# Kernel optimization log

Hardware: AMD Instinct MI355X
Metric: run time of the kernel (lower is better)

Reference implementation:

```python
import jax, jax.numpy as jnp
import numpy as np

N_NODES = 50000


def _glorot(key, fan_in, fan_out):
    limit = float(np.sqrt(6.0 / (fan_in + fan_out)))
    return jax.random.uniform(key, (fan_in, fan_out), jnp.float32, -limit, limit)


def setup_inputs() -> dict:
    key = jax.random.key(0)
    k_x, k_src, k_dst, k1, k2, k3 = jax.random.split(key, 6)
    x = jax.random.normal(k_x, (N_NODES, 128), dtype=jnp.float32)
    src = jax.random.randint(k_src, (800000,), 0, N_NODES)
    dst = jax.random.randint(k_dst, (800000,), 0, N_NODES)
    edge_index = jnp.stack([src, dst]).astype(jnp.int64)  # [2, E]
    W1 = _glorot(k1, 128, 96)
    W2 = _glorot(k2, 96, 96)
    W3 = _glorot(k3, 96, 40)
    b1 = jnp.zeros((96,), jnp.float32)
    b2 = jnp.zeros((96,), jnp.float32)
    b3 = jnp.zeros((40,), jnp.float32)
    return {"x": x, "W1": W1, "b1": b1, "W2": W2, "b2": b2,
            "W3": W3, "b3": b3, "edge_index": edge_index}


def _aggregate(x, src, dst):
    # sparse adj SpMM with 'add' reduce: out[dst] += x[src]
    return jax.ops.segment_sum(x[src], dst, num_segments=N_NODES)


def reference(x, W1, b1, W2, b2, W3, b3, edge_index):
    src, dst = edge_index[0], edge_index[1]
    # layer 1: aggregate -> linear -> relu (dropout identity in eval)
    h = jax.nn.relu(_aggregate(x, src, dst) @ W1 + b1)
    # layer 2
    h = jax.nn.relu(_aggregate(h, src, dst) @ W2 + b2)
    # layer 3 + log_softmax
    logits = _aggregate(h, src, dst) @ W3 + b3
    return jax.nn.log_softmax(logits, axis=-1)
```

## Files before the change

kernel.cpp:

```cpp
#include <hip/hip_runtime.h>
#include <math.h>

typedef __attribute__((ext_vector_type(8))) short bf16x8;
typedef __attribute__((ext_vector_type(4))) float f32x4;

__device__ __forceinline__ unsigned short f2bf(float f) {
  unsigned u = __float_as_uint(f);
  u += 0x7fffu + ((u >> 16) & 1u);
  return (unsigned short)(u >> 16);
}
__device__ __forceinline__ float bflo(unsigned u) { return __uint_as_float(u << 16); }
__device__ __forceinline__ float bfhi(unsigned u) { return __uint_as_float(u & 0xffff0000u); }


constexpr int CB = 64;

__global__ __launch_bounds__(256) void bucket_count(const int* __restrict__ dst,
                                                    int* __restrict__ partial, int E) {
  __shared__ int bkt[256];
  int tid = threadIdx.x;
  bkt[tid] = 0;
  __syncthreads();
  int E4 = E >> 2;
  const int4* d4 = (const int4*)dst;
  for (int i = blockIdx.x * 256 + tid; i < E4; i += gridDim.x * 256) {
    int4 d = d4[i];
    atomicAdd(&bkt[d.x >> 8], 1);
    atomicAdd(&bkt[d.y >> 8], 1);
    atomicAdd(&bkt[d.z >> 8], 1);
    atomicAdd(&bkt[d.w >> 8], 1);
  }
  if (blockIdx.x == 0 && tid < (E & 3)) atomicAdd(&bkt[dst[E4 * 4 + tid] >> 8], 1);
  __syncthreads();
  partial[blockIdx.x * 256 + tid] = bkt[tid];
}

__global__ __launch_bounds__(256) void scan_pack(const int* __restrict__ partial,
                                                 int* __restrict__ gstart, int* __restrict__ gcur,
                                                 int* __restrict__ row_ptr,
                                                 const float* __restrict__ W1,
                                                 const float* __restrict__ W2,
                                                 const float* __restrict__ W3,
                                                 unsigned short* __restrict__ Wp1,
                                                 unsigned short* __restrict__ Wp2,
                                                 unsigned short* __restrict__ Wp3,
                                                 int NB, int N, int E) {
  if (blockIdx.x == 0) {
    int tid = threadIdx.x;
    int s = 0;
#pragma unroll 8
    for (int i = 0; i < CB; ++i) s += partial[i * 256 + tid];
    __shared__ int sm[256];
    sm[tid] = s;
    __syncthreads();
    for (int off = 1; off < 256; off <<= 1) {
      int u = (tid >= off) ? sm[tid - off] : 0;
      __syncthreads();
      sm[tid] += u;
      __syncthreads();
    }
    int excl = sm[tid] - s;
    if (tid < NB) { gstart[tid] = excl; gcur[tid] = excl; }
    if (tid == NB - 1) gstart[NB] = sm[tid];
    if (tid == 0) row_ptr[N] = E;
    return;
  }
  int gid = (blockIdx.x - 1) * 256 + threadIdx.x;
  const float* W;
  unsigned short* Wp;
  int t, NCTT, M, MV;
  if (gid < 1536) {
    W = W1; Wp = Wp1; t = gid; NCTT = 6; M = 96; MV = 96;
  } else if (gid < 2688) {
    W = W2; Wp = Wp2; t = gid - 1536; NCTT = 6; M = 96; MV = 96;
  } else if (gid < 3264) {
    W = W3; Wp = Wp3; t = gid - 2688; NCTT = 3; M = 40; MV = 40;
  } else {
    return;
  }
  int lane = t & 63;
  int frag = t >> 6;
  int s = frag / NCTT;
  int ct = frag - s * NCTT;
  int colv = ct * 16 + (lane & 15);
  int k0 = s * 32 + (lane >> 4) * 8;
  union { unsigned short s[8]; uint4 u; } pk;
#pragma unroll
  for (int j = 0; j < 8; ++j) {
    float v = (colv < MV) ? W[(k0 + j) * M + colv] : 0.f;
    pk.s[j] = f2bf(v);
  }
  ((uint4*)Wp)[t] = pk.u;
}

__global__ __launch_bounds__(512) void bin_edges(const int* __restrict__ src,
                                                 const int* __restrict__ dst,
                                                 int* __restrict__ gcur,
                                                 int* __restrict__ packed, int E, int NB) {
  __shared__ int lcnt[256];
  __shared__ int gbase[256];
  int tid = threadIdx.x;
  if (tid < 256) lcnt[tid] = 0;
  __syncthreads();
  int idx = blockIdx.x * 512 + tid;
  int E4 = E >> 2;
  int sv[4], dv[4], lv[4];
  int cnt = 0;
  if (idx < E4) {
    int4 s4 = ((const int4*)src)[idx];
    int4 d4 = ((const int4*)dst)[idx];
    sv[0] = s4.x; sv[1] = s4.y; sv[2] = s4.z; sv[3] = s4.w;
    dv[0] = d4.x; dv[1] = d4.y; dv[2] = d4.z; dv[3] = d4.w;
    cnt = 4;
  } else if (idx == E4 && (E & 3)) {
    int tl = E & 3;
    for (int i = 0; i < tl; ++i) { sv[i] = src[E4 * 4 + i]; dv[i] = dst[E4 * 4 + i]; }
    cnt = tl;
  }
  for (int i = 0; i < cnt; ++i) lv[i] = atomicAdd(&lcnt[dv[i] >> 8], 1);
  __syncthreads();
  if (tid < NB) gbase[tid] = atomicAdd(&gcur[tid], lcnt[tid]);
  __syncthreads();
  for (int i = 0; i < cnt; ++i) {
    int b = dv[i] >> 8;
    packed[gbase[b] + lv[i]] = ((dv[i] & 255) << 16) | (sv[i] & 0xffff);
  }
}

__global__ __launch_bounds__(256) void build_local_csr(const int* __restrict__ packed,
                                                       const int* __restrict__ gstart,
                                                       int* __restrict__ row_ptr,
                                                       int* __restrict__ col, int N) {
  __shared__ int cnt[256];
  __shared__ int sm[256];
  int b = blockIdx.x, tid = threadIdx.x;
  int gs = gstart[b], ge = gstart[b + 1];
  int me = ge - gs;
  int node0 = b << 8;
  int RL = N - node0;
  if (RL > 256) RL = 256;
  cnt[tid] = 0;
  __syncthreads();
  for (int i = tid; i < me; i += 256) atomicAdd(&cnt[packed[gs + i] >> 16], 1);
  __syncthreads();
  int v = cnt[tid];
  sm[tid] = v;
  __syncthreads();
  for (int off = 1; off < 256; off <<= 1) {
    int u = (tid >= off) ? sm[tid - off] : 0;
    __syncthreads();
    sm[tid] += u;
    __syncthreads();
  }
  int excl = gs + sm[tid] - v;
  __syncthreads();
  cnt[tid] = excl;
  if (tid < RL) row_ptr[node0 + tid] = excl;
  __syncthreads();
  for (int i = tid; i < me; i += 256) {
    int pk = packed[gs + i];
    int p = atomicAdd(&cnt[pk >> 16], 1);
    col[p] = pk & 0xffff;
  }
}


template <int KSTEPS, int NCTT, bool AF32, bool OUTBF16, int MOUT, int MVALID>
__global__ __launch_bounds__(256) void mfma_gemm(const void* __restrict__ Aptr,
                                                 const unsigned short* __restrict__ Wp,
                                                 void* __restrict__ outp, int N) {
  constexpr int NCT = 3;
  constexpr int K = KSTEPS * 32;
  int wid = threadIdx.x >> 6;
  int lane = threadIdx.x & 63;
  int rt = blockIdx.x * 4 + wid;
  if (rt * 16 >= N) return;
  int g = blockIdx.y;
  int quad = lane >> 4;
  int lm = lane & 15;

  union BU { uint4 u; bf16x8 v; };
  bf16x8 bfrag[KSTEPS][NCT];
  const uint4* wp4 = (const uint4*)Wp;
#pragma unroll
  for (int s = 0; s < KSTEPS; ++s)
#pragma unroll
    for (int c = 0; c < NCT; ++c) {
      BU bu;
      bu.u = wp4[(s * NCTT + g * NCT + c) * 64 + lane];
      bfrag[s][c] = bu.v;
    }

  f32x4 acc[NCT];
#pragma unroll
  for (int c = 0; c < NCT; ++c) acc[c] = (f32x4){0.f, 0.f, 0.f, 0.f};

  int row = rt * 16 + lm;
  if (row >= N) row = N - 1;

#pragma unroll
  for (int s = 0; s < KSTEPS; ++s) {
    int k0 = s * 32 + quad * 8;
    bf16x8 afrag;
    if (AF32) {
      const float* Af = (const float*)Aptr + (size_t)row * K + k0;
      float4 x0 = *(const float4*)(Af);
      float4 x1 = *(const float4*)(Af + 4);
      union { unsigned short s[8]; bf16x8 v; } au;
      au.s[0] = f2bf(x0.x); au.s[1] = f2bf(x0.y); au.s[2] = f2bf(x0.z); au.s[3] = f2bf(x0.w);
      au.s[4] = f2bf(x1.x); au.s[5] = f2bf(x1.y); au.s[6] = f2bf(x1.z); au.s[7] = f2bf(x1.w);
      afrag = au.v;
    } else {
      const unsigned short* Ab = (const unsigned short*)Aptr + (size_t)row * K + k0;
      BU au;
      au.u = *(const uint4*)Ab;
      afrag = au.v;
    }
#pragma unroll
    for (int c = 0; c < NCT; ++c)
      acc[c] = __builtin_amdgcn_mfma_f32_16x16x32_bf16(afrag, bfrag[s][c], acc[c], 0, 0, 0);
  }

#pragma unroll
  for (int c = 0; c < NCT; ++c) {
    int colv = g * 48 + c * 16 + lm;
    if (colv >= MVALID) continue;
#pragma unroll
    for (int r = 0; r < 4; ++r) {
      int orow = rt * 16 + quad * 4 + r;
      if (orow < N) {
        if (OUTBF16)
          ((unsigned short*)outp)[(size_t)orow * MOUT + colv] = f2bf(acc[c][r]);
        else
          ((float*)outp)[(size_t)orow * MOUT + colv] = acc[c][r];
      }
    }
  }
}


__global__ void agg_relu_bf16(const unsigned short* __restrict__ t,
                              const int* __restrict__ row_ptr, const int* __restrict__ col,
                              const float* __restrict__ bias, unsigned short* __restrict__ out,
                              int N) {
  int gid = blockIdx.x * blockDim.x + threadIdx.x;
  int node = gid / 12;
  int c = gid - node * 12;
  if (node >= N) return;
  int beg = row_ptr[node];
  int end = row_ptr[node + 1];
  const unsigned short* tc = t + 8 * c;
  float a0 = 0.f, a1 = 0.f, a2 = 0.f, a3 = 0.f, a4 = 0.f, a5 = 0.f, a6 = 0.f, a7 = 0.f;
  int e = beg;
  for (; e + 1 < end; e += 2) {
    int s0 = col[e], s1 = col[e + 1];
    uint4 u = *(const uint4*)(tc + (size_t)s0 * 96);
    uint4 w = *(const uint4*)(tc + (size_t)s1 * 96);
    a0 += bflo(u.x); a1 += bfhi(u.x);
    a2 += bflo(u.y); a3 += bfhi(u.y);
    a4 += bflo(u.z); a5 += bfhi(u.z);
    a6 += bflo(u.w); a7 += bfhi(u.w);
    a0 += bflo(w.x); a1 += bfhi(w.x);
    a2 += bflo(w.y); a3 += bfhi(w.y);
    a4 += bflo(w.z); a5 += bfhi(w.z);
    a6 += bflo(w.w); a7 += bfhi(w.w);
  }
  if (e < end) {
    int s = col[e];
    uint4 u = *(const uint4*)(tc + (size_t)s * 96);
    a0 += bflo(u.x); a1 += bfhi(u.x);
    a2 += bflo(u.y); a3 += bfhi(u.y);
    a4 += bflo(u.z); a5 += bfhi(u.z);
    a6 += bflo(u.w); a7 += bfhi(u.w);
  }
  const float* b = bias + 8 * c;
  union { unsigned short s[8]; uint4 u; } pk;
  pk.s[0] = f2bf(fmaxf(a0 + b[0], 0.f));
  pk.s[1] = f2bf(fmaxf(a1 + b[1], 0.f));
  pk.s[2] = f2bf(fmaxf(a2 + b[2], 0.f));
  pk.s[3] = f2bf(fmaxf(a3 + b[3], 0.f));
  pk.s[4] = f2bf(fmaxf(a4 + b[4], 0.f));
  pk.s[5] = f2bf(fmaxf(a5 + b[5], 0.f));
  pk.s[6] = f2bf(fmaxf(a6 + b[6], 0.f));
  pk.s[7] = f2bf(fmaxf(a7 + b[7], 0.f));
  *(uint4*)(out + (size_t)node * 96 + 8 * c) = pk.u;
}

__global__ void agg_lsm_bf16(const unsigned short* __restrict__ t,
                             const int* __restrict__ row_ptr, const int* __restrict__ col,
                             const float* __restrict__ bias, float* __restrict__ out, int N) {
  int tid = threadIdx.x;
  int node = blockIdx.x * 16 + (tid >> 4);
  int c = tid & 15;
  bool act = (c < 10) && (node < N);
  int ceff = (c < 10) ? c : 0;
  int beg = 0, end = 0;
  if (node < N) {
    beg = row_ptr[node];
    end = row_ptr[node + 1];
  }
  const unsigned short* tc = t + 4 * ceff;
  float v0 = 0.f, v1 = 0.f, v2 = 0.f, v3 = 0.f;
  if (act) {
    int e = beg;
    for (; e + 1 < end; e += 2) {
      int s0 = col[e], s1 = col[e + 1];
      uint2 u = *(const uint2*)(tc + (size_t)s0 * 40);
      uint2 w = *(const uint2*)(tc + (size_t)s1 * 40);
      v0 += bflo(u.x); v1 += bfhi(u.x);
      v2 += bflo(u.y); v3 += bfhi(u.y);
      v0 += bflo(w.x); v1 += bfhi(w.x);
      v2 += bflo(w.y); v3 += bfhi(w.y);
    }
    if (e < end) {
      int s = col[e];
      uint2 u = *(const uint2*)(tc + (size_t)s * 40);
      v0 += bflo(u.x); v1 += bfhi(u.x);
      v2 += bflo(u.y); v3 += bfhi(u.y);
    }
  }
  const float* bb = bias + 4 * ceff;
  v0 += bb[0]; v1 += bb[1]; v2 += bb[2]; v3 += bb[3];
  float m = act ? fmaxf(fmaxf(v0, v1), fmaxf(v2, v3)) : -__builtin_inff();
#pragma unroll
  for (int off = 8; off; off >>= 1) m = fmaxf(m, __shfl_xor(m, off, 64));
  float ex = act ? (__expf(v0 - m) + __expf(v1 - m) + __expf(v2 - m) + __expf(v3 - m)) : 0.f;
#pragma unroll
  for (int off = 8; off; off >>= 1) ex += __shfl_xor(ex, off, 64);
  if (act) {
    float l = m + __logf(ex);
    float* o = out + (size_t)node * 40 + 4 * c;
    o[0] = v0 - l; o[1] = v1 - l; o[2] = v2 - l; o[3] = v3 - l;
  }
}


extern "C" void kernel_launch(void* const* d_in, const int* in_sizes, int n_in,
                              void* d_out, int out_size, void* d_ws, size_t ws_size,
                              hipStream_t stream) {
  const float* x  = (const float*)d_in[0];
  const float* W1 = (const float*)d_in[1];
  const float* b1 = (const float*)d_in[2];
  const float* W2 = (const float*)d_in[3];
  const float* b2 = (const float*)d_in[4];
  const float* W3 = (const float*)d_in[5];
  const float* b3 = (const float*)d_in[6];
  const int* edge = (const int*)d_in[7];

  int N = in_sizes[0] / 128;
  int E = in_sizes[7] / 2;
  const int* srcp = edge;
  const int* dstp = edge + E;

  char* p = (char*)d_ws;
  auto alloc = [&](size_t bytes) {
    char* r = p;
    p += (bytes + 255) & ~size_t(255);
    return r;
  };
  int NB = (N + 255) >> 8;
  int* partial = (int*)alloc((size_t)CB * 256 * 4);
  int* gstart  = (int*)alloc((size_t)(NB + 1) * 4);
  int* gcur    = (int*)alloc((size_t)NB * 4);
  int* row_ptr = (int*)alloc((size_t)(N + 1) * 4);
  int* packed  = (int*)alloc((size_t)E * 4);
  int* col     = (int*)alloc((size_t)E * 4);
  unsigned short* Wp1 = (unsigned short*)alloc(1536 * 8 * 2);
  unsigned short* Wp2 = (unsigned short*)alloc(1152 * 8 * 2);
  unsigned short* Wp3 = (unsigned short*)alloc(576 * 8 * 2);
  unsigned short* Tb  = (unsigned short*)alloc((size_t)N * 96 * 2);
  unsigned short* Hb  = (unsigned short*)alloc((size_t)N * 96 * 2);
  unsigned short* T3b = (unsigned short*)alloc((size_t)N * 40 * 2);

  bucket_count<<<CB, 256, 0, stream>>>(dstp, partial, E);
  scan_pack<<<14, 256, 0, stream>>>(partial, gstart, gcur, row_ptr,
                                    W1, W2, W3, Wp1, Wp2, Wp3, NB, N, E);
  int E4 = E >> 2;
  int nbin = (E4 + ((E & 3) ? 1 : 0) + 511) / 512;
  bin_edges<<<nbin, 512, 0, stream>>>(srcp, dstp, gcur, packed, E, NB);
  build_local_csr<<<NB, 256, 0, stream>>>(packed, gstart, row_ptr, col, N);

  int rt4 = ((N + 15) / 16 + 3) / 4;
  int aggblocks = (N * 12 + 255) / 256;

  mfma_gemm<4, 6, true, true, 96, 96><<<dim3(rt4, 2), 256, 0, stream>>>(x, Wp1, Tb, N);
  agg_relu_bf16<<<aggblocks, 256, 0, stream>>>(Tb, row_ptr, col, b1, Hb, N);
  mfma_gemm<3, 6, false, true, 96, 96><<<dim3(rt4, 2), 256, 0, stream>>>(Hb, Wp2, Tb, N);
  agg_relu_bf16<<<aggblocks, 256, 0, stream>>>(Tb, row_ptr, col, b2, Hb, N);
  mfma_gemm<3, 3, false, true, 40, 40><<<dim3(rt4, 1), 256, 0, stream>>>(Hb, Wp3, T3b, N);
  agg_lsm_bf16<<<(N + 15) / 16, 256, 0, stream>>>(T3b, row_ptr, col, b3, (float*)d_out, N);
}
```

Measured before the change: 219.6 us.

## Fuse aggregation with next-layer GEMM and merge graph-build kernels with GEMM1

```diff
diff --git a/kernel.cpp b/kernel.cpp
--- a/kernel.cpp
+++ b/kernel.cpp
@@ -15,57 +15,34 @@
 
 constexpr int CB = 64;
 
-__global__ __launch_bounds__(256) void bucket_count(const int* __restrict__ dst,
-                                                    int* __restrict__ partial, int E) {
-  __shared__ int bkt[256];
+__global__ __launch_bounds__(256) void count_pack(const int* __restrict__ dst,
+                                                  int* __restrict__ partial, int E,
+                                                  const float* __restrict__ W1,
+                                                  const float* __restrict__ W2,
+                                                  const float* __restrict__ W3,
+                                                  unsigned short* __restrict__ Wp1,
+                                                  unsigned short* __restrict__ Wp2,
+                                                  unsigned short* __restrict__ Wp3) {
   int tid = threadIdx.x;
-  bkt[tid] = 0;
-  __syncthreads();
-  int E4 = E >> 2;
-  const int4* d4 = (const int4*)dst;
-  for (int i = blockIdx.x * 256 + tid; i < E4; i += gridDim.x * 256) {
-    int4 d = d4[i];
-    atomicAdd(&bkt[d.x >> 8], 1);
-    atomicAdd(&bkt[d.y >> 8], 1);
-    atomicAdd(&bkt[d.z >> 8], 1);
-    atomicAdd(&bkt[d.w >> 8], 1);
-  }
-  if (blockIdx.x == 0 && tid < (E & 3)) atomicAdd(&bkt[dst[E4 * 4 + tid] >> 8], 1);
-  __syncthreads();
-  partial[blockIdx.x * 256 + tid] = bkt[tid];
-}
-
-__global__ __launch_bounds__(256) void scan_pack(const int* __restrict__ partial,
-                                                 int* __restrict__ gstart, int* __restrict__ gcur,
-                                                 int* __restrict__ row_ptr,
-                                                 const float* __restrict__ W1,
-                                                 const float* __restrict__ W2,
-                                                 const float* __restrict__ W3,
-                                                 unsigned short* __restrict__ Wp1,
-                                                 unsigned short* __restrict__ Wp2,
-                                                 unsigned short* __restrict__ Wp3,
-                                                 int NB, int N, int E) {
-  if (blockIdx.x == 0) {
-    int tid = threadIdx.x;
-    int s = 0;
-#pragma unroll 8
-    for (int i = 0; i < CB; ++i) s += partial[i * 256 + tid];
-    __shared__ int sm[256];
-    sm[tid] = s;
-    __syncthreads();
-    for (int off = 1; off < 256; off <<= 1) {
-      int u = (tid >= off) ? sm[tid - off] : 0;
-      __syncthreads();
-      sm[tid] += u;
-      __syncthreads();
-    }
-    int excl = sm[tid] - s;
-    if (tid < NB) { gstart[tid] = excl; gcur[tid] = excl; }
-    if (tid == NB - 1) gstart[NB] = sm[tid];
-    if (tid == 0) row_ptr[N] = E;
+  if (blockIdx.x < CB) {
+    __shared__ int bkt[256];
+    bkt[tid] = 0;
+    __syncthreads();
+    int E4 = E >> 2;
+    const int4* d4 = (const int4*)dst;
+    for (int i = blockIdx.x * 256 + tid; i < E4; i += CB * 256) {
+      int4 d = d4[i];
+      atomicAdd(&bkt[d.x >> 8], 1);
+      atomicAdd(&bkt[d.y >> 8], 1);
+      atomicAdd(&bkt[d.z >> 8], 1);
+      atomicAdd(&bkt[d.w >> 8], 1);
+    }
+    if (blockIdx.x == 0 && tid < (E & 3)) atomicAdd(&bkt[dst[E4 * 4 + tid] >> 8], 1);
+    __syncthreads();
+    partial[blockIdx.x * 256 + tid] = bkt[tid];
     return;
   }
-  int gid = (blockIdx.x - 1) * 256 + threadIdx.x;
+  int gid = (blockIdx.x - CB) * 256 + tid;
   const float* W;
   unsigned short* Wp;
   int t, NCTT, M, MV;
@@ -93,37 +70,112 @@
   ((uint4*)Wp)[t] = pk.u;
 }
 
-__global__ __launch_bounds__(512) void bin_edges(const int* __restrict__ src,
+__global__ __launch_bounds__(256) void scan_kernel(const int* __restrict__ partial,
+                                                   int* __restrict__ gstart,
+                                                   int* __restrict__ gcur,
+                                                   int* __restrict__ row_ptr,
+                                                   int NB, int N, int E) {
+  int tid = threadIdx.x;
+  int s = 0;
+#pragma unroll 8
+  for (int i = 0; i < CB; ++i) s += partial[i * 256 + tid];
+  __shared__ int sm[256];
+  sm[tid] = s;
+  __syncthreads();
+  for (int off = 1; off < 256; off <<= 1) {
+    int u = (tid >= off) ? sm[tid - off] : 0;
+    __syncthreads();
+    sm[tid] += u;
+    __syncthreads();
+  }
+  int excl = sm[tid] - s;
+  if (tid < NB) { gstart[tid] = excl; gcur[tid] = excl; }
+  if (tid == NB - 1) gstart[NB] = sm[tid];
+  if (tid == 0) row_ptr[N] = E;
+}
+
+__global__ __launch_bounds__(256) void bin_gemm1(const int* __restrict__ src,
                                                  const int* __restrict__ dst,
                                                  int* __restrict__ gcur,
-                                                 int* __restrict__ packed, int E, int NB) {
-  __shared__ int lcnt[256];
-  __shared__ int gbase[256];
+                                                 int* __restrict__ packed, int E, int NB,
+                                                 int NBIN, const float* __restrict__ x,
+                                                 const unsigned short* __restrict__ Wp1,
+                                                 unsigned short* __restrict__ Tb, int N) {
   int tid = threadIdx.x;
-  if (tid < 256) lcnt[tid] = 0;
-  __syncthreads();
-  int idx = blockIdx.x * 512 + tid;
-  int E4 = E >> 2;
-  int sv[4], dv[4], lv[4];
-  int cnt = 0;
-  if (idx < E4) {
-    int4 s4 = ((const int4*)src)[idx];
-    int4 d4 = ((const int4*)dst)[idx];
-    sv[0] = s4.x; sv[1] = s4.y; sv[2] = s4.z; sv[3] = s4.w;
-    dv[0] = d4.x; dv[1] = d4.y; dv[2] = d4.z; dv[3] = d4.w;
-    cnt = 4;
-  } else if (idx == E4 && (E & 3)) {
-    int tl = E & 3;
-    for (int i = 0; i < tl; ++i) { sv[i] = src[E4 * 4 + i]; dv[i] = dst[E4 * 4 + i]; }
-    cnt = tl;
-  }
-  for (int i = 0; i < cnt; ++i) lv[i] = atomicAdd(&lcnt[dv[i] >> 8], 1);
-  __syncthreads();
-  if (tid < NB) gbase[tid] = atomicAdd(&gcur[tid], lcnt[tid]);
-  __syncthreads();
-  for (int i = 0; i < cnt; ++i) {
-    int b = dv[i] >> 8;
-    packed[gbase[b] + lv[i]] = ((dv[i] & 255) << 16) | (sv[i] & 0xffff);
+  if (blockIdx.x < NBIN) {
+    __shared__ int lcnt[256];
+    __shared__ int gbase[256];
+    lcnt[tid] = 0;
+    __syncthreads();
+    int idx = blockIdx.x * 256 + tid;
+    int E4 = E >> 2;
+    int sv[4], dv[4], lv[4];
+    int cnt = 0;
+    if (idx < E4) {
+      int4 s4 = ((const int4*)src)[idx];
+      int4 d4 = ((const int4*)dst)[idx];
+      sv[0] = s4.x; sv[1] = s4.y; sv[2] = s4.z; sv[3] = s4.w;
+      dv[0] = d4.x; dv[1] = d4.y; dv[2] = d4.z; dv[3] = d4.w;
+      cnt = 4;
+    } else if (idx == E4 && (E & 3)) {
+      int tl = E & 3;
+      for (int i = 0; i < tl; ++i) { sv[i] = src[E4 * 4 + i]; dv[i] = dst[E4 * 4 + i]; }
+      cnt = tl;
+    }
+    for (int i = 0; i < cnt; ++i) lv[i] = atomicAdd(&lcnt[dv[i] >> 8], 1);
+    __syncthreads();
+    if (tid < NB) gbase[tid] = atomicAdd(&gcur[tid], lcnt[tid]);
+    __syncthreads();
+    for (int i = 0; i < cnt; ++i) {
+      int b = dv[i] >> 8;
+      packed[gbase[b] + lv[i]] = ((dv[i] & 255) << 16) | (sv[i] & 0xffff);
+    }
+    return;
+  }
+  int bx = blockIdx.x - NBIN;
+  int wid = tid >> 6;
+  int lane = tid & 63;
+  int rt = bx * 4 + wid;
+  if (rt * 16 >= N) return;
+  int quad = lane >> 4;
+  int lm = lane & 15;
+  union BU { uint4 u; bf16x8 v; };
+  bf16x8 bfrag[4][6];
+  const uint4* wp4 = (const uint4*)Wp1;
+#pragma unroll
+  for (int s = 0; s < 4; ++s)
+#pragma unroll
+    for (int c = 0; c < 6; ++c) {
+      BU bu;
+      bu.u = wp4[(s * 6 + c) * 64 + lane];
+      bfrag[s][c] = bu.v;
+    }
+  f32x4 acc[6];
+#pragma unroll
+  for (int c = 0; c < 6; ++c) acc[c] = (f32x4){0.f, 0.f, 0.f, 0.f};
+  int row = rt * 16 + lm;
+  if (row >= N) row = N - 1;
+#pragma unroll
+  for (int s = 0; s < 4; ++s) {
+    int k0 = s * 32 + quad * 8;
+    const float* Af = x + (size_t)row * 128 + k0;
+    float4 x0 = *(const float4*)(Af);
+    float4 x1 = *(const float4*)(Af + 4);
+    union { unsigned short s[8]; bf16x8 v; } au;
+    au.s[0] = f2bf(x0.x); au.s[1] = f2bf(x0.y); au.s[2] = f2bf(x0.z); au.s[3] = f2bf(x0.w);
+    au.s[4] = f2bf(x1.x); au.s[5] = f2bf(x1.y); au.s[6] = f2bf(x1.z); au.s[7] = f2bf(x1.w);
+#pragma unroll
+    for (int c = 0; c < 6; ++c)
+      acc[c] = __builtin_amdgcn_mfma_f32_16x16x32_bf16(au.v, bfrag[s][c], acc[c], 0, 0, 0);
+  }
+#pragma unroll
+  for (int c = 0; c < 6; ++c) {
+    int colv = c * 16 + lm;
+#pragma unroll
+    for (int r = 0; r < 4; ++r) {
+      int orow = rt * 16 + quad * 4 + r;
+      if (orow < N) Tb[(size_t)orow * 96 + colv] = f2bf(acc[c][r]);
+    }
   }
 }
 
@@ -165,125 +217,104 @@
 }
 
 
-template <int KSTEPS, int NCTT, bool AF32, bool OUTBF16, int MOUT, int MVALID>
-__global__ __launch_bounds__(256) void mfma_gemm(const void* __restrict__ Aptr,
-                                                 const unsigned short* __restrict__ Wp,
-                                                 void* __restrict__ outp, int N) {
-  constexpr int NCT = 3;
-  constexpr int K = KSTEPS * 32;
-  int wid = threadIdx.x >> 6;
-  int lane = threadIdx.x & 63;
-  int rt = blockIdx.x * 4 + wid;
-  if (rt * 16 >= N) return;
-  int g = blockIdx.y;
+template <int NCT, int MOUT, int MVALID>
+__global__ __launch_bounds__(256) void fused_agg_gemm(const unsigned short* __restrict__ tin,
+                                                      const int* __restrict__ row_ptr,
+                                                      const int* __restrict__ col,
+                                                      const float* __restrict__ bias,
+                                                      const unsigned short* __restrict__ Wp,
+                                                      unsigned short* __restrict__ outp, int N) {
+  constexpr int LST = 104;
+  __shared__ unsigned short sH[64 * LST];
+  int tid = threadIdx.x;
+  int node0 = blockIdx.x * 64;
+
+#pragma unroll
+  for (int it = 0; it < 3; ++it) {
+    int u = tid + it * 256;
+    int nl = u / 12;
+    int c = u - nl * 12;
+    int node = node0 + nl;
+    if (node < N) {
+      int beg = row_ptr[node];
+      int end = row_ptr[node + 1];
+      const unsigned short* tc = tin + 8 * c;
+      float a0 = 0.f, a1 = 0.f, a2 = 0.f, a3 = 0.f, a4 = 0.f, a5 = 0.f, a6 = 0.f, a7 = 0.f;
+      int e = beg;
+      for (; e + 1 < end; e += 2) {
+        int s0 = col[e], s1 = col[e + 1];
+        uint4 u4 = *(const uint4*)(tc + (size_t)s0 * 96);
+        uint4 w4 = *(const uint4*)(tc + (size_t)s1 * 96);
+        a0 += bflo(u4.x); a1 += bfhi(u4.x);
+        a2 += bflo(u4.y); a3 += bfhi(u4.y);
+        a4 += bflo(u4.z); a5 += bfhi(u4.z);
+        a6 += bflo(u4.w); a7 += bfhi(u4.w);
+        a0 += bflo(w4.x); a1 += bfhi(w4.x);
+        a2 += bflo(w4.y); a3 += bfhi(w4.y);
+        a4 += bflo(w4.z); a5 += bfhi(w4.z);
+        a6 += bflo(w4.w); a7 += bfhi(w4.w);
+      }
+      if (e < end) {
+        int s0 = col[e];
+        uint4 u4 = *(const uint4*)(tc + (size_t)s0 * 96);
+        a0 += bflo(u4.x); a1 += bfhi(u4.x);
+        a2 += bflo(u4.y); a3 += bfhi(u4.y);
+        a4 += bflo(u4.z); a5 += bfhi(u4.z);
+        a6 += bflo(u4.w); a7 += bfhi(u4.w);
+      }
+      const float* b = bias + 8 * c;
+      union { unsigned short s[8]; uint4 u; } pk;
+      pk.s[0] = f2bf(fmaxf(a0 + b[0], 0.f));
+      pk.s[1] = f2bf(fmaxf(a1 + b[1], 0.f));
+      pk.s[2] = f2bf(fmaxf(a2 + b[2], 0.f));
+      pk.s[3] = f2bf(fmaxf(a3 + b[3], 0.f));
+      pk.s[4] = f2bf(fmaxf(a4 + b[4], 0.f));
+      pk.s[5] = f2bf(fmaxf(a5 + b[5], 0.f));
+      pk.s[6] = f2bf(fmaxf(a6 + b[6], 0.f));
+      pk.s[7] = f2bf(fmaxf(a7 + b[7], 0.f));
+      *(uint4*)&sH[nl * LST + c * 8] = pk.u;
+    }
+  }
+  __syncthreads();
+
+  int wid = tid >> 6;
+  int lane = tid & 63;
+  int rt16 = wid * 16;
+  if (node0 + rt16 >= N) return;
   int quad = lane >> 4;
   int lm = lane & 15;
-
   union BU { uint4 u; bf16x8 v; };
-  bf16x8 bfrag[KSTEPS][NCT];
+  bf16x8 bfrag[3][NCT];
   const uint4* wp4 = (const uint4*)Wp;
 #pragma unroll
-  for (int s = 0; s < KSTEPS; ++s)
+  for (int s = 0; s < 3; ++s)
 #pragma unroll
     for (int c = 0; c < NCT; ++c) {
       BU bu;
-      bu.u = wp4[(s * NCTT + g * NCT + c) * 64 + lane];
+      bu.u = wp4[(s * NCT + c) * 64 + lane];
       bfrag[s][c] = bu.v;
     }
-
   f32x4 acc[NCT];
 #pragma unroll
   for (int c = 0; c < NCT; ++c) acc[c] = (f32x4){0.f, 0.f, 0.f, 0.f};
-
-  int row = rt * 16 + lm;
-  if (row >= N) row = N - 1;
-
-#pragma unroll
-  for (int s = 0; s < KSTEPS; ++s) {
-    int k0 = s * 32 + quad * 8;
-    bf16x8 afrag;
-    if (AF32) {
-      const float* Af = (const float*)Aptr + (size_t)row * K + k0;
-      float4 x0 = *(const float4*)(Af);
-      float4 x1 = *(const float4*)(Af + 4);
-      union { unsigned short s[8]; bf16x8 v; } au;
-      au.s[0] = f2bf(x0.x); au.s[1] = f2bf(x0.y); au.s[2] = f2bf(x0.z); au.s[3] = f2bf(x0.w);
-      au.s[4] = f2bf(x1.x); au.s[5] = f2bf(x1.y); au.s[6] = f2bf(x1.z); au.s[7] = f2bf(x1.w);
-      afrag = au.v;
-    } else {
-      const unsigned short* Ab = (const unsigned short*)Aptr + (size_t)row * K + k0;
-      BU au;
-      au.u = *(const uint4*)Ab;
-      afrag = au.v;
-    }
+#pragma unroll
+  for (int s = 0; s < 3; ++s) {
+    BU au;
+    au.u = *(const uint4*)&sH[(rt16 + lm) * LST + s * 32 + quad * 8];
 #pragma unroll
     for (int c = 0; c < NCT; ++c)
-      acc[c] = __builtin_amdgcn_mfma_f32_16x16x32_bf16(afrag, bfrag[s][c], acc[c], 0, 0, 0);
-  }
-
+      acc[c] = __builtin_amdgcn_mfma_f32_16x16x32_bf16(au.v, bfrag[s][c], acc[c], 0, 0, 0);
+  }
 #pragma unroll
   for (int c = 0; c < NCT; ++c) {
-    int colv = g * 48 + c * 16 + lm;
+    int colv = c * 16 + lm;
     if (colv >= MVALID) continue;
 #pragma unroll
     for (int r = 0; r < 4; ++r) {
-      int orow = rt * 16 + quad * 4 + r;
-      if (orow < N) {
-        if (OUTBF16)
-          ((unsigned short*)outp)[(size_t)orow * MOUT + colv] = f2bf(acc[c][r]);
-        else
-          ((float*)outp)[(size_t)orow * MOUT + colv] = acc[c][r];
-      }
-    }
-  }
-}
-
-
-__global__ void agg_relu_bf16(const unsigned short* __restrict__ t,
-                              const int* __restrict__ row_ptr, const int* __restrict__ col,
-                              const float* __restrict__ bias, unsigned short* __restrict__ out,
-                              int N) {
-  int gid = blockIdx.x * blockDim.x + threadIdx.x;
-  int node = gid / 12;
-  int c = gid - node * 12;
-  if (node >= N) return;
-  int beg = row_ptr[node];
-  int end = row_ptr[node + 1];
-  const unsigned short* tc = t + 8 * c;
-  float a0 = 0.f, a1 = 0.f, a2 = 0.f, a3 = 0.f, a4 = 0.f, a5 = 0.f, a6 = 0.f, a7 = 0.f;
-  int e = beg;
-  for (; e + 1 < end; e += 2) {
-    int s0 = col[e], s1 = col[e + 1];
-    uint4 u = *(const uint4*)(tc + (size_t)s0 * 96);
-    uint4 w = *(const uint4*)(tc + (size_t)s1 * 96);
-    a0 += bflo(u.x); a1 += bfhi(u.x);
-    a2 += bflo(u.y); a3 += bfhi(u.y);
-    a4 += bflo(u.z); a5 += bfhi(u.z);
-    a6 += bflo(u.w); a7 += bfhi(u.w);
-    a0 += bflo(w.x); a1 += bfhi(w.x);
-    a2 += bflo(w.y); a3 += bfhi(w.y);
-    a4 += bflo(w.z); a5 += bfhi(w.z);
-    a6 += bflo(w.w); a7 += bfhi(w.w);
-  }
-  if (e < end) {
-    int s = col[e];
-    uint4 u = *(const uint4*)(tc + (size_t)s * 96);
-    a0 += bflo(u.x); a1 += bfhi(u.x);
-    a2 += bflo(u.y); a3 += bfhi(u.y);
-    a4 += bflo(u.z); a5 += bfhi(u.z);
-    a6 += bflo(u.w); a7 += bfhi(u.w);
-  }
-  const float* b = bias + 8 * c;
-  union { unsigned short s[8]; uint4 u; } pk;
-  pk.s[0] = f2bf(fmaxf(a0 + b[0], 0.f));
-  pk.s[1] = f2bf(fmaxf(a1 + b[1], 0.f));
-  pk.s[2] = f2bf(fmaxf(a2 + b[2], 0.f));
-  pk.s[3] = f2bf(fmaxf(a3 + b[3], 0.f));
-  pk.s[4] = f2bf(fmaxf(a4 + b[4], 0.f));
-  pk.s[5] = f2bf(fmaxf(a5 + b[5], 0.f));
-  pk.s[6] = f2bf(fmaxf(a6 + b[6], 0.f));
-  pk.s[7] = f2bf(fmaxf(a7 + b[7], 0.f));
-  *(uint4*)(out + (size_t)node * 96 + 8 * c) = pk.u;
+      int orow = node0 + rt16 + quad * 4 + r;
+      if (orow < N) outp[(size_t)orow * MOUT + colv] = f2bf(acc[c][r]);
+    }
+  }
 }
 
 __global__ void agg_lsm_bf16(const unsigned short* __restrict__ t,
@@ -313,8 +344,8 @@
       v2 += bflo(w.y); v3 += bfhi(w.y);
     }
     if (e < end) {
-      int s = col[e];
-      uint2 u = *(const uint2*)(tc + (size_t)s * 40);
+      int s0 = col[e];
+      uint2 u = *(const uint2*)(tc + (size_t)s0 * 40);
       v0 += bflo(u.x); v1 += bfhi(u.x);
       v2 += bflo(u.y); v3 += bfhi(u.y);
     }
@@ -369,24 +400,20 @@
   unsigned short* Wp2 = (unsigned short*)alloc(1152 * 8 * 2);
   unsigned short* Wp3 = (unsigned short*)alloc(576 * 8 * 2);
   unsigned short* Tb  = (unsigned short*)alloc((size_t)N * 96 * 2);
-  unsigned short* Hb  = (unsigned short*)alloc((size_t)N * 96 * 2);
+  unsigned short* T2b = (unsigned short*)alloc((size_t)N * 96 * 2);
   unsigned short* T3b = (unsigned short*)alloc((size_t)N * 40 * 2);
 
-  bucket_count<<<CB, 256, 0, stream>>>(dstp, partial, E);
-  scan_pack<<<14, 256, 0, stream>>>(partial, gstart, gcur, row_ptr,
-                                    W1, W2, W3, Wp1, Wp2, Wp3, NB, N, E);
   int E4 = E >> 2;
-  int nbin = (E4 + ((E & 3) ? 1 : 0) + 511) / 512;
-  bin_edges<<<nbin, 512, 0, stream>>>(srcp, dstp, gcur, packed, E, NB);
+  int nbin = (E4 + ((E & 3) ? 1 : 0) + 255) / 256;
+  int GB = ((N + 15) / 16 + 3) / 4;
+  int FB = (N + 63) / 64;
+
+  count_pack<<<CB + 13, 256, 0, stream>>>(dstp, partial, E, W1, W2, W3, Wp1, Wp2, Wp3);
+  scan_kernel<<<1, 256, 0, stream>>>(partial, gstart, gcur, row_ptr, NB, N, E);
+  bin_gemm1<<<nbin + GB, 256, 0, stream>>>(srcp, dstp, gcur, packed, E, NB, nbin,
+                                           x, Wp1, Tb, N);
   build_local_csr<<<NB, 256, 0, stream>>>(packed, gstart, row_ptr, col, N);
-
-  int rt4 = ((N + 15) / 16 + 3) / 4;
-  int aggblocks = (N * 12 + 255) / 256;
-
-  mfma_gemm<4, 6, true, true, 96, 96><<<dim3(rt4, 2), 256, 0, stream>>>(x, Wp1, Tb, N);
-  agg_relu_bf16<<<aggblocks, 256, 0, stream>>>(Tb, row_ptr, col, b1, Hb, N);
-  mfma_gemm<3, 6, false, true, 96, 96><<<dim3(rt4, 2), 256, 0, stream>>>(Hb, Wp2, Tb, N);
-  agg_relu_bf16<<<aggblocks, 256, 0, stream>>>(Tb, row_ptr, col, b2, Hb, N);
-  mfma_gemm<3, 3, false, true, 40, 40><<<dim3(rt4, 1), 256, 0, stream>>>(Hb, Wp3, T3b, N);
+  fused_agg_gemm<6, 96, 96><<<FB, 256, 0, stream>>>(Tb, row_ptr, col, b1, Wp2, T2b, N);
+  fused_agg_gemm<3, 40, 40><<<FB, 256, 0, stream>>>(T2b, row_ptr, col, b2, Wp3, T3b, N);
   agg_lsm_bf16<<<(N + 15) / 16, 256, 0, stream>>>(T3b, row_ptr, col, b3, (float*)d_out, N);
 }
```

New measurement: 223.0 us. Within noise of the previous version (+1.6%).
